# Optimization experiments

Measured on AMD Instinct MI355X. Metric: run time of the kernel, lower is better.

The kernel has to match this reference:

```python
import jax, jax.numpy as jnp
import numpy as np

D_MODEL = 1024
NUM_HEADS = 16
D_K = D_MODEL // NUM_HEADS
THETA = 10000.0
BATCH = 2
SEQ = 2048


def apply_rope(x, token_positions):
    # x: [B, H, S, D_K]; token_positions: [S] int
    half = D_K // 2
    inv_freq = THETA ** (-(jnp.arange(half, dtype=jnp.float32) * 2.0) / D_K)  # [half]
    angles = token_positions.astype(jnp.float32)[:, None] * inv_freq[None, :]  # [S, half]
    cos = jnp.cos(angles)  # [S, half]
    sin = jnp.sin(angles)
    x1 = x[..., 0::2]  # even indices
    x2 = x[..., 1::2]  # odd indices
    out_even = x1 * cos - x2 * sin
    out_odd = x1 * sin + x2 * cos
    # interleave back: [..., S, half, 2] -> [..., S, D_K]
    return jnp.stack([out_even, out_odd], axis=-1).reshape(x.shape)


def setup_inputs() -> dict:
    key = jax.random.key(0)
    ks = jax.random.split(key, 5)
    x = jax.random.normal(ks[0], (BATCH, SEQ, D_MODEL), dtype=jnp.float32)
    token_positions = jnp.arange(SEQ, dtype=jnp.int64)
    scale = 0.02
    Wq = jax.random.normal(ks[1], (D_MODEL, D_MODEL), dtype=jnp.float32) * scale
    Wk = jax.random.normal(ks[2], (D_MODEL, D_MODEL), dtype=jnp.float32) * scale
    Wv = jax.random.normal(ks[3], (D_MODEL, D_MODEL), dtype=jnp.float32) * scale
    Wo = jax.random.normal(ks[4], (D_MODEL, D_MODEL), dtype=jnp.float32) * scale
    return {"x": x, "token_positions": token_positions, "Wq": Wq, "Wk": Wk, "Wv": Wv, "Wo": Wo}


def reference(x, token_positions, Wq, Wk, Wv, Wo):
    B, S, _ = x.shape
    # cs336 Linear: y = x @ W.T with W of shape (out, in), no bias
    def proj(W):
        h = jnp.einsum('bsd,od->bso', x, W)
        return h.reshape(B, S, NUM_HEADS, D_K).transpose(0, 2, 1, 3)  # [B,H,S,Dk]
    Q = apply_rope(proj(Wq), token_positions)
    K = apply_rope(proj(Wk), token_positions)
    V = proj(Wv)
    scores = jnp.einsum('bhqd,bhkd->bhqk', Q, K) / jnp.sqrt(jnp.float32(D_K))
    causal = jnp.tril(jnp.ones((S, S), dtype=bool))
    scores = jnp.where(causal, scores, -jnp.inf)
    attn = jax.nn.softmax(scores, axis=-1)
    out = jnp.einsum('bhqk,bhkd->bhqd', attn, V)  # [B,H,S,Dk]
    out = out.transpose(0, 2, 1, 3).reshape(B, S, D_MODEL)
    return jnp.einsum('bsd,od->bso', out, Wo)
```

## Files before the change

kernel.cpp:

```cpp
#include <hip/hip_runtime.h>
#include <hip/hip_bf16.h>
#include <math.h>

#define NHEADS 16
#define DKH 64
#define SEQ 2048
#define DMODEL 1024

typedef __attribute__((ext_vector_type(8))) short short8;
typedef __attribute__((ext_vector_type(4))) float f32x4;

#define GLDS16(g, l)                                         \
  __builtin_amdgcn_global_load_lds(                          \
      (__attribute__((address_space(1))) void*)(void*)(g),   \
      (__attribute__((address_space(3))) void*)(l), 16, 0, 0)

__device__ __forceinline__ short f2bf(float f) {
  unsigned u = __float_as_uint(f);
  unsigned r = (u + 0x7fffu + ((u >> 16) & 1u)) >> 16;
  return (short)r;
}

__device__ __forceinline__ unsigned cvtpk(float lo, float hi) {
  unsigned r;
  asm("v_cvt_pk_bf16_f32 %0, %1, %2" : "=v"(r) : "v"(lo), "v"(hi));
  return r;
}

__device__ __forceinline__ short8 pack8(float4 a, float4 b) {
  short8 v;
  v[0] = f2bf(a.x); v[1] = f2bf(a.y); v[2] = f2bf(a.z); v[3] = f2bf(a.w);
  v[4] = f2bf(b.x); v[5] = f2bf(b.y); v[6] = f2bf(b.z); v[7] = f2bf(b.w);
  return v;
}

__device__ __forceinline__ int swz(int r, int gran) {
  return r * 64 + ((gran ^ (r & 7)) << 3);
}

__global__ __launch_bounds__(256) void precast_rope_kernel(
    const float* __restrict__ X, const float* __restrict__ Wq,
    const float* __restrict__ Wk, const float* __restrict__ Wv,
    const float* __restrict__ Wo, const int* __restrict__ tp,
    short* __restrict__ Xb, short* __restrict__ Wqb, short* __restrict__ Wkb,
    short* __restrict__ Wvb, short* __restrict__ Wob,
    float* __restrict__ ct, float* __restrict__ st) {
  int bid = blockIdx.x;
  if (bid < 4096) {
    int i = bid * 256 + threadIdx.x;
    const float* src; short* dst; int off;
    if (i < 524288) { src = X; dst = Xb; off = i; }
    else {
      int k = i - 524288; int w = k >> 17; off = k & 131071;
      src = (w == 0) ? Wq : (w == 1) ? Wk : (w == 2) ? Wv : Wo;
      dst = (w == 0) ? Wqb : (w == 1) ? Wkb : (w == 2) ? Wvb : Wob;
    }
    const float4* p = reinterpret_cast<const float4*>(src) + 2 * (size_t)off;
    float4 a = p[0], b = p[1];
    reinterpret_cast<short8*>(dst)[off] = pack8(a, b);
  } else {
    int idx = (bid - 4096) * 256 + threadIdx.x;
    if (idx >= SEQ * 32) return;
    int s = idx >> 5, i = idx & 31;
    int is64 = (tp[1] == 0);
    int p = is64 ? tp[2 * s] : tp[s];
    float invf = powf(10000.0f, -(2.0f * (float)i) / 64.0f);
    float a = (float)p * invf;
    ct[idx] = cosf(a);
    st[idx] = sinf(a);
  }
}

__global__ __launch_bounds__(512, 2) void gemm_qkv_kernel(
    const short* __restrict__ X, const short* __restrict__ Wq,
    const short* __restrict__ Wk, const short* __restrict__ Wv,
    short* __restrict__ Qb, short* __restrict__ Kb, short* __restrict__ Vb,
    const float* __restrict__ ct, const float* __restrict__ st) {
  __shared__ __align__(16) short As[2][256 * 64];
  __shared__ __align__(16) short Bs[2][192 * 64];
  const int id = blockIdx.x;
  const int xcd = id & 7, rr = id >> 3;
  const int tm = (xcd & 3) * 4 + (rr & 3);
  const int tn = (xcd >> 2) * 8 + (rr >> 2);
  const int tid = threadIdx.x;
  const int wave = tid >> 6, lane = tid & 63;
  const int l15 = lane & 15, quad = lane >> 4;
  const int wm = wave >> 2, wn = wave & 3;

  const int n0 = tn * 192;
  const short* Abase = X + (size_t)(tm * 256) * DMODEL;
  const short* Bbase = Wq + (size_t)n0 * DMODEL;
  (void)Wk; (void)Wv;

  const int lr = lane >> 3;
  const int lc = (lane & 7) ^ lr;

#define STGA(bufi, half, kt_)                                              \
  do {                                                                     \
    int R0 = (half) * 128 + wave * 16;                                     \
    GLDS16(Abase + (size_t)(R0 + lr) * DMODEL + (kt_) * 64 + lc * 8,       \
           &As[bufi][R0 * 64 + lane * 8]);                                 \
    GLDS16(Abase + (size_t)(R0 + 8 + lr) * DMODEL + (kt_) * 64 + lc * 8,   \
           &As[bufi][(R0 + 8) * 64 + lane * 8]);                           \
  } while (0)
#define STGB(bufi, t, kt_)                                                 \
  do {                                                                     \
    int R0 = (t) * 64 + wave * 8;                                          \
    GLDS16(Bbase + (size_t)(R0 + lr) * DMODEL + (kt_) * 64 + lc * 8,       \
           &Bs[bufi][R0 * 64 + lane * 8]);                                 \
  } while (0)

  f32x4 acc[8][3];
#pragma unroll
  for (int m = 0; m < 8; m++)
#pragma unroll
    for (int n = 0; n < 3; n++) acc[m][n] = (f32x4){0.f, 0.f, 0.f, 0.f};

  STGB(0, 0, 0); STGB(0, 1, 0); STGB(0, 2, 0);
  STGA(0, 0, 0); STGA(0, 1, 0);
  STGB(1, 0, 1); STGB(1, 1, 1); STGB(1, 2, 1);

  short8 bfr[3][2];
  for (int kt = 0; kt < 16; kt++) {
    const int buf = kt & 1;
    if (kt < 15) { STGA(buf ^ 1, 0, kt + 1); }
    if (kt < 15) { asm volatile("s_waitcnt vmcnt(5)" ::: "memory"); }
    else         { asm volatile("s_waitcnt vmcnt(0)" ::: "memory"); }
    asm volatile("s_barrier" ::: "memory");
#pragma unroll
    for (int nb = 0; nb < 3; nb++)
#pragma unroll
      for (int ks = 0; ks < 2; ks++)
        bfr[nb][ks] = *reinterpret_cast<const short8*>(
            &Bs[buf][swz(wn * 48 + nb * 16 + l15, ks * 4 + quad)]);
    {
      short8 af[2][2];
#pragma unroll
      for (int j = 0; j < 2; j++)
#pragma unroll
        for (int ks = 0; ks < 2; ks++)
          af[j][ks] = *reinterpret_cast<const short8*>(
              &As[buf][swz(wm * 128 + j * 16 + l15, ks * 4 + quad)]);
      __builtin_amdgcn_s_setprio(1);
#pragma unroll
      for (int j = 0; j < 2; j++)
#pragma unroll
        for (int nb = 0; nb < 3; nb++)
#pragma unroll
          for (int ks = 0; ks < 2; ks++)
            acc[j][nb] = __builtin_amdgcn_mfma_f32_16x16x32_bf16(
                af[j][ks], bfr[nb][ks], acc[j][nb], 0, 0, 0);
      __builtin_amdgcn_s_setprio(0);
    }
    asm volatile("s_barrier" ::: "memory");
#pragma unroll
    for (int p = 1; p < 4; p++) {
      short8 af[2][2];
#pragma unroll
      for (int j = 0; j < 2; j++)
#pragma unroll
        for (int ks = 0; ks < 2; ks++)
          af[j][ks] = *reinterpret_cast<const short8*>(
              &As[buf][swz(wm * 128 + (p * 2 + j) * 16 + l15, ks * 4 + quad)]);
      if (p == 1)      { if (kt < 15) { STGA(buf ^ 1, 1, kt + 1); } }
      else if (p == 2) { if (kt < 14) { STGB(buf, 0, kt + 2); STGB(buf, 1, kt + 2); } }
      else             { if (kt < 14) { STGB(buf, 2, kt + 2); } }
      asm volatile("s_barrier" ::: "memory");
      __builtin_amdgcn_s_setprio(1);
#pragma unroll
      for (int j = 0; j < 2; j++)
#pragma unroll
        for (int nb = 0; nb < 3; nb++)
#pragma unroll
          for (int ks = 0; ks < 2; ks++)
            acc[p * 2 + j][nb] = __builtin_amdgcn_mfma_f32_16x16x32_bf16(
                af[j][ks], bfr[nb][ks], acc[p * 2 + j][nb], 0, 0, 0);
      __builtin_amdgcn_s_setprio(0);
      asm volatile("s_barrier" ::: "memory");
    }
  }
#undef STGA
#undef STGB

#pragma unroll
  for (int mf = 0; mf < 8; mf++) {
    const int s0g = tm * 256 + wm * 128 + mf * 16 + quad * 4;
    const int b = s0g >> 11, s = s0g & 2047;
#pragma unroll
    for (int nb = 0; nb < 3; nb++) {
      int nl = n0 + wn * 48 + nb * 16 + l15;
      int mid = nl >> 10;
      int c = nl & 1023;
      int h = c >> 6, dd = c & 63;
      if (mid == 2) {
        unsigned u0 = (unsigned)(unsigned short)f2bf(acc[mf][nb][0]) |
                      ((unsigned)(unsigned short)f2bf(acc[mf][nb][1]) << 16);
        unsigned u1 = (unsigned)(unsigned short)f2bf(acc[mf][nb][2]) |
                      ((unsigned)(unsigned short)f2bf(acc[mf][nb][3]) << 16);
        uint2 pk; pk.x = u0; pk.y = u1;
        *reinterpret_cast<uint2*>(Vb + ((size_t)(b * NHEADS + h) * DKH + dd) * SEQ + s) = pk;
      } else {
#pragma unroll
        for (int reg = 0; reg < 4; reg++) {
          float v = acc[mf][nb][reg];
          float pv = __shfl_xor(v, 1);
          int fi = dd >> 1;
          int sg = s + reg;
          float cc = ct[sg * 32 + fi], sn = st[sg * 32 + fi];
          float o = (dd & 1) ? (pv * sn + v * cc) : (v * cc - pv * sn);
          size_t oi = (((size_t)(b * NHEADS + h)) * SEQ + sg) * DKH + dd;
          ((mid == 0) ? Qb : Kb)[oi] = f2bf(o);
        }
      }
    }
  }
}

__global__ __launch_bounds__(256, 4) void attn_kernel(
    const short* __restrict__ Qb, const short* __restrict__ Kb,
    const short* __restrict__ Vtb, short* __restrict__ Ob) {
  __shared__ __align__(16) short Ks[2][64 * 64];
  __shared__ __align__(16) short Vs[2][64 * 64];

  const int id = blockIdx.x;
  const int x8 = id & 7;
  const int c  = (id >> 3) & 31;
  const int q2 = id >> 8;
  const int bh = x8 * 4 + q2;
  const int qt = (q2 == 0) ? c
               : (q2 == 1) ? (31 - c)
               : (q2 == 2) ? ((c + 16) & 31)
               : ((15 - c) & 31);

  const int tid = threadIdx.x;
  const int wave = tid >> 6, lane = tid & 63;
  const int l15 = lane & 15, quad = lane >> 4;
  const int sr0 = tid >> 3, sc = tid & 7;

  const int vga = ((sc >> 2) << 2) + ((sc & 1) << 1);
  const int vh4 = ((sc >> 1) & 1) * 4;

  const short* Qp = Qb + (size_t)bh * SEQ * DKH;
  const short* Kp = Kb + (size_t)bh * SEQ * DKH;
  const short* Vp = Vtb + (size_t)bh * DKH * SEQ;

  uint4 kreg[2], vreg[2];
#pragma unroll
  for (int i = 0; i < 2; i++) {
    int r = sr0 + i * 32;
    kreg[i] = *reinterpret_cast<const uint4*>(Kp + (size_t)r * DKH + sc * 8);
    vreg[i] = *reinterpret_cast<const uint4*>(Vp + (size_t)r * SEQ + sc * 8);
  }
  short8 qf0, qf1;
  {
    const short* qrow = Qp + (size_t)(qt * 64 + wave * 16 + l15) * DKH;
    qf0 = *reinterpret_cast<const short8*>(qrow + quad * 8);
    qf1 = *reinterpret_cast<const short8*>(qrow + (4 + quad) * 8);
  }
#pragma unroll
  for (int i = 0; i < 2; i++) {
    int r = sr0 + i * 32;
    *reinterpret_cast<uint4*>(&Ks[0][swz(r, sc)]) = kreg[i];
    uint2 lo, hi;
    lo.x = vreg[i].x; lo.y = vreg[i].y; hi.x = vreg[i].z; hi.y = vreg[i].w;
    *reinterpret_cast<uint2*>(&Vs[0][swz(r, vga) + vh4]) = lo;
    *reinterpret_cast<uint2*>(&Vs[0][swz(r, vga + 1) + vh4]) = hi;
  }
  __syncthreads();

  f32x4 accO[4];
#pragma unroll
  for (int i = 0; i < 4; i++) accO[i] = (f32x4){0.f, 0.f, 0.f, 0.f};
  float rs = 0.f;

  const float SCL = 0.125f * 1.44269504089f;
  const float FM = 13.0f;

  int buf = 0;
  for (int kt = 0; kt <= qt; kt++) {
    if (kt < qt) {
#pragma unroll
      for (int i = 0; i < 2; i++) {
        int r = sr0 + i * 32;
        kreg[i] = *reinterpret_cast<const uint4*>(Kp + (size_t)((kt + 1) * 64 + r) * DKH + sc * 8);
        vreg[i] = *reinterpret_cast<const uint4*>(Vp + (size_t)r * SEQ + (kt + 1) * 64 + sc * 8);
      }
    }

    f32x4 sa[4];
    __builtin_amdgcn_s_setprio(1);
#pragma unroll
    for (int nb = 0; nb < 4; nb++) {
      sa[nb] = (f32x4){0.f, 0.f, 0.f, 0.f};
      int r = nb * 16 + l15;
      short8 kf0 = *reinterpret_cast<const short8*>(&Ks[buf][swz(r, quad)]);
      sa[nb] = __builtin_amdgcn_mfma_f32_16x16x32_bf16(kf0, qf0, sa[nb], 0, 0, 0);
      short8 kf1 = *reinterpret_cast<const short8*>(&Ks[buf][swz(r, 4 + quad)]);
      sa[nb] = __builtin_amdgcn_mfma_f32_16x16x32_bf16(kf1, qf1, sa[nb], 0, 0, 0);
    }
    __builtin_amdgcn_s_setprio(0);

    const bool diag = (kt == qt);
    const int prow = wave * 16 + l15;
    unsigned pu[4], pw[4];
#pragma unroll
    for (int nb = 0; nb < 4; nb++) {
      float p0 = exp2f(sa[nb][0] * SCL - FM);
      float p1 = exp2f(sa[nb][1] * SCL - FM);
      float p2 = exp2f(sa[nb][2] * SCL - FM);
      float p3 = exp2f(sa[nb][3] * SCL - FM);
      if (diag) {
        int kbase = nb * 16 + quad * 4;
        if (kbase + 0 > prow) p0 = 0.f;
        if (kbase + 1 > prow) p1 = 0.f;
        if (kbase + 2 > prow) p2 = 0.f;
        if (kbase + 3 > prow) p3 = 0.f;
      }
      rs += (p0 + p1) + (p2 + p3);
      pu[nb] = cvtpk(p0, p1);
      pw[nb] = cvtpk(p2, p3);
    }

    short8 pf0, pf1;
    {
      unsigned* w0 = reinterpret_cast<unsigned*>(&pf0);
      w0[0] = pu[0]; w0[1] = pw[0]; w0[2] = pu[1]; w0[3] = pw[1];
      unsigned* w1 = reinterpret_cast<unsigned*>(&pf1);
      w1[0] = pu[2]; w1[1] = pw[2]; w1[2] = pu[3]; w1[3] = pw[3];
    }
    __builtin_amdgcn_s_setprio(1);
#pragma unroll
    for (int db = 0; db < 4; db++) {
      int dv = db * 16 + l15;
      short8 vf0 = *reinterpret_cast<const short8*>(&Vs[buf][swz(dv, quad)]);
      accO[db] = __builtin_amdgcn_mfma_f32_16x16x32_bf16(pf0, vf0, accO[db], 0, 0, 0);
      short8 vf1 = *reinterpret_cast<const short8*>(&Vs[buf][swz(dv, 4 + quad)]);
      accO[db] = __builtin_amdgcn_mfma_f32_16x16x32_bf16(pf1, vf1, accO[db], 0, 0, 0);
    }
    __builtin_amdgcn_s_setprio(0);

    if (kt < qt) {
      int nbuf = buf ^ 1;
#pragma unroll
      for (int i = 0; i < 2; i++) {
        int r = sr0 + i * 32;
        *reinterpret_cast<uint4*>(&Ks[nbuf][swz(r, sc)]) = kreg[i];
        uint2 lo, hi;
        lo.x = vreg[i].x; lo.y = vreg[i].y; hi.x = vreg[i].z; hi.y = vreg[i].w;
        *reinterpret_cast<uint2*>(&Vs[nbuf][swz(r, vga) + vh4]) = lo;
        *reinterpret_cast<uint2*>(&Vs[nbuf][swz(r, vga + 1) + vh4]) = hi;
      }
      __syncthreads();
      buf = nbuf;
    }
  }

  float t = rs;
  t += __shfl_xor(t, 16);
  t += __shfl_xor(t, 32);
  float lv[4];
#pragma unroll
  for (int reg = 0; reg < 4; reg++) lv[reg] = __shfl(t, quad * 4 + reg);

  int b = bh >> 4, h = bh & 15;
#pragma unroll
  for (int db = 0; db < 4; db++)
#pragma unroll
    for (int reg = 0; reg < 4; reg++) {
      int s = qt * 64 + wave * 16 + quad * 4 + reg;
      int dv = db * 16 + l15;
      float o = accO[db][reg] / lv[reg];
      Ob[((size_t)(b * SEQ + s)) * DMODEL + h * DKH + dv] = f2bf(o);
    }
}

__global__ __launch_bounds__(256) void gemm_out_kernel(
    const short* __restrict__ X, const short* __restrict__ Wo, float* __restrict__ Out) {
  __shared__ __align__(16) short As[128 * 64];
  __shared__ __align__(16) short Bs[64 * 64];
  const int tm = blockIdx.x;
  const int tn = blockIdx.y;
  const int tid = threadIdx.x;
  const int wave = tid >> 6, lane = tid & 63;
  const int l15 = lane & 15, quad = lane >> 4;
  const int wm = wave >> 1, wn = wave & 1;

  const short* Abase = X + (size_t)(tm * 128) * DMODEL;
  const short* Bbase = Wo + (size_t)(tn * 64) * DMODEL;

  const int lr = lane >> 3;
  const int lc = (lane & 7) ^ lr;

  f32x4 acc[4][2];
#pragma unroll
  for (int mb = 0; mb < 4; mb++)
#pragma unroll
    for (int nb = 0; nb < 2; nb++) acc[mb][nb] = (f32x4){0.f, 0.f, 0.f, 0.f};

  for (int kk = 0; kk < 16; kk++) {
    const short* Ak = Abase + kk * 64;
    const short* Bk = Bbase + kk * 64;
#pragma unroll
    for (int i = 0; i < 4; i++) {
      int R = i * 32 + wave * 8;
      GLDS16(Ak + (size_t)(R + lr) * DMODEL + lc * 8, &As[R * 64 + lane * 8]);
    }
#pragma unroll
    for (int i = 0; i < 2; i++) {
      int R = i * 32 + wave * 8;
      GLDS16(Bk + (size_t)(R + lr) * DMODEL + lc * 8, &Bs[R * 64 + lane * 8]);
    }
    __syncthreads();
#pragma unroll
    for (int kg = 0; kg < 2; kg++) {
      short8 af[4], bf[2];
#pragma unroll
      for (int mb = 0; mb < 4; mb++) {
        int r = wm * 64 + mb * 16 + l15;
        af[mb] = *reinterpret_cast<const short8*>(&As[swz(r, kg * 4 + quad)]);
      }
#pragma unroll
      for (int nb = 0; nb < 2; nb++) {
        int r = wn * 32 + nb * 16 + l15;
        bf[nb] = *reinterpret_cast<const short8*>(&Bs[swz(r, kg * 4 + quad)]);
      }
#pragma unroll
      for (int mb = 0; mb < 4; mb++)
#pragma unroll
        for (int nb = 0; nb < 2; nb++)
          acc[mb][nb] = __builtin_amdgcn_mfma_f32_16x16x32_bf16(af[mb], bf[nb], acc[mb][nb], 0, 0, 0);
    }
    __syncthreads();
  }
#pragma unroll
  for (int mb = 0; mb < 4; mb++)
#pragma unroll
    for (int nb = 0; nb < 2; nb++)
#pragma unroll
      for (int reg = 0; reg < 4; reg++) {
        int rg = tm * 128 + wm * 64 + mb * 16 + quad * 4 + reg;
        int col = tn * 64 + wn * 32 + nb * 16 + l15;
        Out[(size_t)rg * DMODEL + col] = acc[mb][nb][reg];
      }
}

extern "C" void kernel_launch(void* const* d_in, const int* in_sizes, int n_in,
                              void* d_out, int out_size, void* d_ws, size_t ws_size,
                              hipStream_t stream) {
  (void)in_sizes; (void)n_in; (void)out_size; (void)ws_size;
  const float* X  = (const float*)d_in[0];
  const int*   tp = (const int*)d_in[1];
  const float* Wq = (const float*)d_in[2];
  const float* Wk = (const float*)d_in[3];
  const float* Wv = (const float*)d_in[4];
  const float* Wo = (const float*)d_in[5];
  float* Out = (float*)d_out;

  short* Qb  = (short*)d_ws;
  short* Kb  = Qb + 4194304;
  short* Vb  = Kb + 4194304;
  short* Ab  = Vb + 4194304;
  short* Xb  = Ab + 4194304;
  short* Wqb = Xb + 4194304;
  short* Wkb = Wqb + 1048576;
  short* Wvb = Wkb + 1048576;
  short* Wob = Wvb + 1048576;
  float* ct  = (float*)(Wob + 1048576);
  float* st  = ct + SEQ * 32;

  precast_rope_kernel<<<dim3(4352), dim3(256), 0, stream>>>(
      X, Wq, Wk, Wv, Wo, tp, Xb, Wqb, Wkb, Wvb, Wob, ct, st);
  gemm_qkv_kernel<<<dim3(256), dim3(512), 0, stream>>>(Xb, Wqb, Wkb, Wvb,
                                                       Qb, Kb, Vb, ct, st);
  attn_kernel<<<dim3(1024), dim3(256), 0, stream>>>(Qb, Kb, Vb, Ab);
  gemm_out_kernel<<<dim3(32, 16), dim3(256), 0, stream>>>(Ab, Wob, Out);
}
```

Baseline: 182.8 us.

## Shrink QKV GEMM tile to 128x192 with 4 waves and simpler double buffering

The QKV projection GEMM moves from 256x192 tiles with 8 waves per block (256 blocks) to 128x192 tiles with 4 waves (512 blocks). Each wave now owns a 48-column strip across all 128 rows. The fine-grained interleaved staging with multiple barriers per k-step becomes a plain double-buffered loop: issue the next tile's loads, wait, then compute. The XCD-aware block remapping is dropped in favour of linear indexing. The aim is more blocks for better CU fill and less barrier overhead, at the cost of less A/B reuse per block, more redundant global loads of the weights, and possibly worse L2 locality.

```diff
diff --git a/kernel.cpp b/kernel.cpp
--- a/kernel.cpp
+++ b/kernel.cpp
@@ -71,44 +71,43 @@
   }
 }
 
-__global__ __launch_bounds__(512, 2) void gemm_qkv_kernel(
+__global__ __launch_bounds__(256, 2) void gemm_qkv_kernel(
     const short* __restrict__ X, const short* __restrict__ Wq,
     const short* __restrict__ Wk, const short* __restrict__ Wv,
     short* __restrict__ Qb, short* __restrict__ Kb, short* __restrict__ Vb,
     const float* __restrict__ ct, const float* __restrict__ st) {
-  __shared__ __align__(16) short As[2][256 * 64];
+  __shared__ __align__(16) short As[2][128 * 64];
   __shared__ __align__(16) short Bs[2][192 * 64];
   const int id = blockIdx.x;
-  const int xcd = id & 7, rr = id >> 3;
-  const int tm = (xcd & 3) * 4 + (rr & 3);
-  const int tn = (xcd >> 2) * 8 + (rr >> 2);
+  const int tm = id >> 4;
+  const int tn = id & 15;
   const int tid = threadIdx.x;
   const int wave = tid >> 6, lane = tid & 63;
   const int l15 = lane & 15, quad = lane >> 4;
-  const int wm = wave >> 2, wn = wave & 3;
 
   const int n0 = tn * 192;
-  const short* Abase = X + (size_t)(tm * 256) * DMODEL;
+  const short* Abase = X + (size_t)(tm * 128) * DMODEL;
   const short* Bbase = Wq + (size_t)n0 * DMODEL;
   (void)Wk; (void)Wv;
 
   const int lr = lane >> 3;
   const int lc = (lane & 7) ^ lr;
 
-#define STGA(bufi, half, kt_)                                              \
+#define STG(kt_, bufi)                                                     \
   do {                                                                     \
-    int R0 = (half) * 128 + wave * 16;                                     \
-    GLDS16(Abase + (size_t)(R0 + lr) * DMODEL + (kt_) * 64 + lc * 8,       \
-           &As[bufi][R0 * 64 + lane * 8]);                                 \
-    GLDS16(Abase + (size_t)(R0 + 8 + lr) * DMODEL + (kt_) * 64 + lc * 8,   \
-           &As[bufi][(R0 + 8) * 64 + lane * 8]);                           \
+    _Pragma("unroll")                                                      \
+    for (int i2 = 0; i2 < 4; i2++) {                                       \
+      int R0 = i2 * 32 + wave * 8;                                         \
+      GLDS16(Abase + (size_t)(R0 + lr) * DMODEL + (kt_) * 64 + lc * 8,     \
+             &As[bufi][R0 * 64 + lane * 8]);                               \
+    }                                                                      \
+    _Pragma("unroll")                                                      \
+    for (int i2 = 0; i2 < 6; i2++) {                                       \
+      int R0 = i2 * 32 + wave * 8;                                         \
+      GLDS16(Bbase + (size_t)(R0 + lr) * DMODEL + (kt_) * 64 + lc * 8,     \
+             &Bs[bufi][R0 * 64 + lane * 8]);                               \
+    }                                                                      \
   } while (0)
-#define STGB(bufi, t, kt_)                                                 \
-  do {                                                                     \
-    int R0 = (t) * 64 + wave * 8;                                          \
-    GLDS16(Bbase + (size_t)(R0 + lr) * DMODEL + (kt_) * 64 + lc * 8,       \
-           &Bs[bufi][R0 * 64 + lane * 8]);                                 \
-  } while (0)
 
   f32x4 acc[8][3];
 #pragma unroll
@@ -116,79 +115,44 @@
 #pragma unroll
     for (int n = 0; n < 3; n++) acc[m][n] = (f32x4){0.f, 0.f, 0.f, 0.f};
 
-  STGB(0, 0, 0); STGB(0, 1, 0); STGB(0, 2, 0);
-  STGA(0, 0, 0); STGA(0, 1, 0);
-  STGB(1, 0, 1); STGB(1, 1, 1); STGB(1, 2, 1);
-
-  short8 bfr[3][2];
+  STG(0, 0);
   for (int kt = 0; kt < 16; kt++) {
     const int buf = kt & 1;
-    if (kt < 15) { STGA(buf ^ 1, 0, kt + 1); }
-    if (kt < 15) { asm volatile("s_waitcnt vmcnt(5)" ::: "memory"); }
+    if (kt < 15) { STG(kt + 1, buf ^ 1); }
+    if (kt < 15) { asm volatile("s_waitcnt vmcnt(10)" ::: "memory"); }
     else         { asm volatile("s_waitcnt vmcnt(0)" ::: "memory"); }
     asm volatile("s_barrier" ::: "memory");
 #pragma unroll
-    for (int nb = 0; nb < 3; nb++)
-#pragma unroll
-      for (int ks = 0; ks < 2; ks++)
-        bfr[nb][ks] = *reinterpret_cast<const short8*>(
-            &Bs[buf][swz(wn * 48 + nb * 16 + l15, ks * 4 + quad)]);
-    {
-      short8 af[2][2];
-#pragma unroll
-      for (int j = 0; j < 2; j++)
-#pragma unroll
-        for (int ks = 0; ks < 2; ks++)
-          af[j][ks] = *reinterpret_cast<const short8*>(
-              &As[buf][swz(wm * 128 + j * 16 + l15, ks * 4 + quad)]);
+    for (int ks = 0; ks < 2; ks++) {
+      short8 bfr[3], af[8];
+#pragma unroll
+      for (int nb = 0; nb < 3; nb++)
+        bfr[nb] = *reinterpret_cast<const short8*>(
+            &Bs[buf][swz(wave * 48 + nb * 16 + l15, ks * 4 + quad)]);
+#pragma unroll
+      for (int mf = 0; mf < 8; mf++)
+        af[mf] = *reinterpret_cast<const short8*>(
+            &As[buf][swz(mf * 16 + l15, ks * 4 + quad)]);
       __builtin_amdgcn_s_setprio(1);
 #pragma unroll
-      for (int j = 0; j < 2; j++)
+      for (int mf = 0; mf < 8; mf++)
 #pragma unroll
         for (int nb = 0; nb < 3; nb++)
-#pragma unroll
-          for (int ks = 0; ks < 2; ks++)
-            acc[j][nb] = __builtin_amdgcn_mfma_f32_16x16x32_bf16(
-                af[j][ks], bfr[nb][ks], acc[j][nb], 0, 0, 0);
+          acc[mf][nb] = __builtin_amdgcn_mfma_f32_16x16x32_bf16(
+              af[mf], bfr[nb], acc[mf][nb], 0, 0, 0);
       __builtin_amdgcn_s_setprio(0);
     }
     asm volatile("s_barrier" ::: "memory");
-#pragma unroll
-    for (int p = 1; p < 4; p++) {
-      short8 af[2][2];
-#pragma unroll
-      for (int j = 0; j < 2; j++)
-#pragma unroll
-        for (int ks = 0; ks < 2; ks++)
-          af[j][ks] = *reinterpret_cast<const short8*>(
-              &As[buf][swz(wm * 128 + (p * 2 + j) * 16 + l15, ks * 4 + quad)]);
-      if (p == 1)      { if (kt < 15) { STGA(buf ^ 1, 1, kt + 1); } }
-      else if (p == 2) { if (kt < 14) { STGB(buf, 0, kt + 2); STGB(buf, 1, kt + 2); } }
-      else             { if (kt < 14) { STGB(buf, 2, kt + 2); } }
-      asm volatile("s_barrier" ::: "memory");
-      __builtin_amdgcn_s_setprio(1);
-#pragma unroll
-      for (int j = 0; j < 2; j++)
-#pragma unroll
-        for (int nb = 0; nb < 3; nb++)
-#pragma unroll
-          for (int ks = 0; ks < 2; ks++)
-            acc[p * 2 + j][nb] = __builtin_amdgcn_mfma_f32_16x16x32_bf16(
-                af[j][ks], bfr[nb][ks], acc[p * 2 + j][nb], 0, 0, 0);
-      __builtin_amdgcn_s_setprio(0);
-      asm volatile("s_barrier" ::: "memory");
-    }
-  }
-#undef STGA
-#undef STGB
+  }
+#undef STG
 
 #pragma unroll
   for (int mf = 0; mf < 8; mf++) {
-    const int s0g = tm * 256 + wm * 128 + mf * 16 + quad * 4;
+    const int s0g = tm * 128 + mf * 16 + quad * 4;
     const int b = s0g >> 11, s = s0g & 2047;
 #pragma unroll
     for (int nb = 0; nb < 3; nb++) {
-      int nl = n0 + wn * 48 + nb * 16 + l15;
+      int nl = n0 + wave * 48 + nb * 16 + l15;
       int mid = nl >> 10;
       int c = nl & 1023;
       int h = c >> 6, dd = c & 63;
@@ -470,7 +434,7 @@
 
   precast_rope_kernel<<<dim3(4352), dim3(256), 0, stream>>>(
       X, Wq, Wk, Wv, Wo, tp, Xb, Wqb, Wkb, Wvb, Wob, ct, st);
-  gemm_qkv_kernel<<<dim3(256), dim3(512), 0, stream>>>(Xb, Wqb, Wkb, Wvb,
+  gemm_qkv_kernel<<<dim3(512), dim3(256), 0, stream>>>(Xb, Wqb, Wkb, Wvb,
                                                        Qb, Kb, Vb, ct, st);
   attn_kernel<<<dim3(1024), dim3(256), 0, stream>>>(Qb, Kb, Vb, Ab);
   gemm_out_kernel<<<dim3(32, 16), dim3(256), 0, stream>>>(Ab, Wob, Out);
```

Result: no change. 181.5 us (-0.7%).
